# Kernel optimization log

Hardware: AMD Instinct MI355X
Metric: run time of the kernel (lower is better)

The kernel has to match this reference:

```python
import jax, jax.numpy as jnp
import numpy as np

NUM_HEADS = 8
LN_EPS = 1e-5


def setup_inputs() -> dict:
    key = jax.random.key(0)
    ks = jax.random.split(key, 8)
    B, H, W, C = 2, 64, 64, 256
    return {
        "x": jax.random.normal(ks[0], (B, H, W, C), dtype=jnp.float32),
        "cond": jax.random.normal(ks[1], (B, C), dtype=jnp.float32),
        "t": jax.random.randint(ks[2], (B,), 0, 100, dtype=jnp.int64),
        "emb_table": jax.random.normal(ks[3], (100, C), dtype=jnp.float32) * 0.02,
        "ada_w": jax.random.normal(ks[4], (C, 2 * C), dtype=jnp.float32) * 0.02,
        "ada_b": jnp.zeros((2 * C,), dtype=jnp.float32),
        "qkv_w": jax.random.normal(ks[5], (C, 3 * C), dtype=jnp.float32) * 0.02,
        "qkv_b": jnp.zeros((3 * C,), dtype=jnp.float32),
        "proj_w": jax.random.normal(ks[6], (C, C), dtype=jnp.float32) * 0.02,
        "proj_b": jnp.zeros((C,), dtype=jnp.float32),
    }


def reference(x, cond, t, emb_table, ada_w, ada_b, qkv_w, qkv_b, proj_w, proj_b):
    B, H, W, C = x.shape
    N = H * W
    h = NUM_HEADS
    d = C // h
    scale = d ** -0.5

    x = x.reshape(B, N, C)

    # AdaLayerNorm (adalayernorm_abs): timestep embedding -> SiLU -> Linear -> scale/shift
    emb = emb_table[t]                                # [B, C]
    ss = jax.nn.silu(emb) @ ada_w + ada_b             # [B, 2C]
    sc, sh = jnp.split(ss, 2, axis=-1)                # each [B, C]
    mu = jnp.mean(x, axis=-1, keepdims=True)
    var = jnp.var(x, axis=-1, keepdims=True)
    xn = (x - mu) * jax.lax.rsqrt(var + LN_EPS)       # LN without affine
    x = xn * (1.0 + sc[:, None, :]) + sh[:, None, :]

    # QKV projection and head split
    qkv = (x @ qkv_w + qkv_b).reshape(B, N, 3, h, d)
    qkv = jnp.transpose(qkv, (2, 0, 3, 1, 4))          # [3, B, h, N, d]
    q, k, v = qkv[0], qkv[1], qkv[2]

    # Manual attention: full [B, h, N, N] scores (matches original module)
    attn = jnp.einsum('bhnd,bhmd->bhnm', q, k) * scale
    attn = jax.nn.softmax(attn, axis=-1)
    out = jnp.einsum('bhnm,bhmd->bhnd', attn, v)       # [B, h, N, d]
    out = jnp.transpose(out, (0, 2, 1, 3)).reshape(B, N, C)

    out = (out.reshape(B, H, W, C) @ proj_w) + proj_b
    return out
```

## Files before the change

kernel.cpp:

```cpp
#include <hip/hip_runtime.h>
#include <hip/hip_bf16.h>
#include <stdint.h>

typedef __attribute__((ext_vector_type(8))) short bfrag;
typedef __attribute__((ext_vector_type(4))) short bfrag4;
typedef __attribute__((ext_vector_type(4))) float f32x4;
typedef __attribute__((ext_vector_type(2))) float f32x2;
typedef __attribute__((ext_vector_type(2))) unsigned int u32x2;
typedef __attribute__((ext_vector_type(4))) unsigned int u32x4;

__device__ inline short f2bf(float f) {
  union { float f; uint32_t u; } v; v.f = f;
  uint32_t u = v.u;
  uint32_t r = (u + 0x7fffu + ((u >> 16) & 1u)) >> 16;
  return (short)r;
}
__device__ inline float bf2f(short s) {
  return __builtin_bit_cast(float, (uint32_t)((uint32_t)(uint16_t)s << 16));
}

#if __has_builtin(__builtin_amdgcn_cvt_pk_bf16_f32)
typedef __attribute__((ext_vector_type(2))) __bf16 bf16x2_t;
__device__ inline uint32_t pack_bf16(float a, float b) {
  bf16x2_t r = __builtin_amdgcn_cvt_pk_bf16_f32(a, b);
  return __builtin_bit_cast(uint32_t, r);
}
#else
__device__ inline uint32_t pack_bf16(float a, float b) {
  uint32_t ua = __builtin_bit_cast(uint32_t, a) + 0x8000u;
  uint32_t ub = __builtin_bit_cast(uint32_t, b) + 0x8000u;
  return __builtin_amdgcn_perm(ub, ua, 0x07060302);
}
#endif

__device__ inline void lds_barrier() {
  asm volatile("s_waitcnt lgkmcnt(0)" ::: "memory");
  __builtin_amdgcn_s_barrier();
  asm volatile("" ::: "memory");
}

__global__ __launch_bounds__(256) void prep_kernel(
    const float* __restrict__ emb_table, const int* __restrict__ t,
    const float* __restrict__ ada_w, const float* __restrict__ ada_b,
    float* __restrict__ scsh,
    const float* __restrict__ qkv_w, short* __restrict__ qkv_wt,
    const float* __restrict__ proj_w, short* __restrict__ proj_wt) {
  __shared__ float smem[64 * 65];
  const int blk = blockIdx.x;
  const int tid = threadIdx.x;
  if (blk < 16) {
    float* se = smem;
    float* part = smem + 256;
    int b = blk >> 3, ox = blk & 7;
    int tt = t[b];
    float e = emb_table[tt * 256 + tid];
    se[tid] = e / (1.f + __expf(-e));
    __syncthreads();
    int ol = tid & 63, kc = tid >> 6;
    int o = ox * 64 + ol;
    float acc = 0.f;
#pragma unroll 8
    for (int k = kc * 64; k < (kc + 1) * 64; ++k) acc += se[k] * ada_w[k * 512 + o];
    part[tid] = acc;
    __syncthreads();
    if (tid < 64) {
      int oo = ox * 64 + tid;
      scsh[b * 512 + oo] =
          part[tid] + part[64 + tid] + part[128 + tid] + part[192 + tid] + ada_b[oo];
    }
  } else {
    const float* W; short* Wt; int N, lb;
    if (blk < 64) { W = qkv_w; Wt = qkv_wt; N = 768; lb = blk - 16; }
    else          { W = proj_w; Wt = proj_wt; N = 256; lb = blk - 64; }
    float (*tile)[65] = (float(*)[65])smem;
    int k0 = (lb & 3) * 64, n0 = (lb >> 2) * 64;
    int r = tid >> 2, c0 = (tid & 3) * 16;
    const float* src = W + (long)(k0 + r) * N + n0 + c0;
#pragma unroll
    for (int j = 0; j < 16; j += 4) {
      float4 v = *(const float4*)(src + j);
      tile[r][c0 + j] = v.x; tile[r][c0 + j + 1] = v.y;
      tile[r][c0 + j + 2] = v.z; tile[r][c0 + j + 3] = v.w;
    }
    __syncthreads();
    int nl = tid >> 2, kc = (tid & 3) * 16;
    short outv[16];
#pragma unroll
    for (int j = 0; j < 16; ++j) outv[j] = f2bf(tile[kc + j][nl]);
    short* dst = Wt + (long)(n0 + nl) * 256 + k0 + kc;
    *(bfrag*)dst = *(bfrag*)&outv[0];
    *(bfrag*)(dst + 8) = *(bfrag*)&outv[8];
  }
}

__global__ __launch_bounds__(256) void ln_kernel(const float* __restrict__ x,
                                                 const float* __restrict__ scsh,
                                                 short* __restrict__ xb) {
  int row = blockIdx.x * 4 + (threadIdx.x >> 6);
  int b = row >> 12;
  int lane = threadIdx.x & 63;
  float4 v = *(const float4*)(x + (long)row * 256 + lane * 4);
  float s = v.x + v.y + v.z + v.w;
  float sq = v.x * v.x + v.y * v.y + v.z * v.z + v.w * v.w;
#pragma unroll
  for (int off = 32; off > 0; off >>= 1) {
    s += __shfl_xor(s, off);
    sq += __shfl_xor(sq, off);
  }
  float mu = s * (1.f / 256.f);
  float var = sq * (1.f / 256.f) - mu * mu;
  float rstd = rsqrtf(var + 1e-5f);
  const float* scp = scsh + b * 512 + lane * 4;
  float4 sc = *(const float4*)scp;
  float4 sh = *(const float4*)(scp + 256);
  float y0 = (v.x - mu) * rstd * (1.f + sc.x) + sh.x;
  float y1 = (v.y - mu) * rstd * (1.f + sc.y) + sh.y;
  float y2 = (v.z - mu) * rstd * (1.f + sc.z) + sh.z;
  float y3 = (v.w - mu) * rstd * (1.f + sc.w) + sh.w;
  u32x2 o; o.x = pack_bf16(y0, y1); o.y = pack_bf16(y2, y3);
  *(u32x2*)&xb[(long)row * 256 + lane * 4] = o;
}

__global__ __launch_bounds__(256) void gemm_qkv(const short* __restrict__ A,
                                                const short* __restrict__ Bt,
                                                const float* __restrict__ bias,
                                                float qscale,
                                                short* __restrict__ qk,
                                                short* __restrict__ vT) {
  __shared__ short As[128 * 40];
  __shared__ short Bs[64 * 40];
  const int mt = blockIdx.x, nt = blockIdx.y;
  const int tid = threadIdx.x;
  const int w = tid >> 6, lane = tid & 63, l16 = lane & 15, quad = lane >> 4;
  const int ar = tid >> 1, ak = (tid & 1) * 16;
  const int br = tid >> 2, bk = (tid & 3) * 8;
  f32x4 acc[2][4] = {};
  const short* Arow = A + (long)(mt * 128 + ar) * 256 + ak;
  const short* Brow = Bt + (long)(nt * 64 + br) * 256 + bk;
  bfrag a8a = *(const bfrag*)Arow;
  bfrag a8b = *(const bfrag*)(Arow + 8);
  bfrag b8  = *(const bfrag*)Brow;
  for (int kk = 0; kk < 8; ++kk) {
    __syncthreads();
    *(bfrag*)&As[ar * 40 + ak] = a8a;
    *(bfrag*)&As[ar * 40 + ak + 8] = a8b;
    *(bfrag*)&Bs[br * 40 + bk] = b8;
    __syncthreads();
    int kn = (kk < 7) ? (kk + 1) : 7;
    a8a = *(const bfrag*)(Arow + kn * 32);
    a8b = *(const bfrag*)(Arow + kn * 32 + 8);
    b8  = *(const bfrag*)(Brow + kn * 32);
    bfrag a0 = *(const bfrag*)&As[(w * 32 + l16) * 40 + quad * 8];
    bfrag a1 = *(const bfrag*)&As[(w * 32 + 16 + l16) * 40 + quad * 8];
#pragma unroll
    for (int c = 0; c < 4; ++c) {
      bfrag bf = *(const bfrag*)&Bs[(c * 16 + l16) * 40 + quad * 8];
      acc[0][c] = __builtin_amdgcn_mfma_f32_16x16x32_bf16(a0, bf, acc[0][c], 0, 0, 0);
      acc[1][c] = __builtin_amdgcn_mfma_f32_16x16x32_bf16(a1, bf, acc[1][c], 0, 0, 0);
    }
  }
  const int rowb = mt * 128 + w * 32 + quad * 4;
  if (nt < 8) {
#pragma unroll
    for (int rg = 0; rg < 2; ++rg) {
      int row0 = rowb + rg * 16;
#pragma unroll
      for (int c = 0; c < 4; ++c) {
        int col = nt * 64 + c * 16 + l16;
        float bv = bias[col];
        float mult = (col < 256) ? qscale : 1.0f;
#pragma unroll
        for (int r = 0; r < 4; ++r)
          qk[(long)(row0 + r) * 512 + col] = f2bf((acc[rg][c][r] + bv) * mult);
      }
    }
  } else {
    const int bb = mt >> 5;
#pragma unroll
    for (int rg = 0; rg < 2; ++rg) {
      int keyl = (rowb + rg * 16) & 4095;
#pragma unroll
      for (int c = 0; c < 4; ++c) {
        int col = nt * 64 + c * 16 + l16;
        float bv = bias[col];
        int d = col - 512;
        u32x2 dd;
        dd.x = pack_bf16(acc[rg][c][0] + bv, acc[rg][c][1] + bv);
        dd.y = pack_bf16(acc[rg][c][2] + bv, acc[rg][c][3] + bv);
        *(u32x2*)&vT[((long)(bb * 8 + (d >> 5)) * 32 + (d & 31)) * 4096 + keyl] = dd;
      }
    }
  }
}

__global__ __launch_bounds__(256) void attn_kernel(const short* __restrict__ qk,
                                                   const short* __restrict__ vT,
                                                   short* __restrict__ OpB,
                                                   float* __restrict__ lpart) {
  const int bid = blockIdx.x;
  const int c = bid & 7, j = bid >> 3;
  const int bh = c * 2 + (j >> 7);
  const int qt = j & 31;
  const int ks = (j >> 5) & 3;
  const int b = bh >> 3, hh = bh & 7;
  const int tid = threadIdx.x;
  const int w = tid >> 6, lane = tid & 63, l16 = lane & 15, quad = lane >> 4;
  const int sig0 = ((l16 >> 2) * 8) + (l16 & 3);

  __shared__ short Ks[2][128 * 36];
  __shared__ short Vt[2][32 * 132];

  const long rowbase = (long)b * 4096;
  const int qrow0 = qt * 128 + w * 32 + l16;
  bfrag qf[2];
#pragma unroll
  for (int g = 0; g < 2; ++g)
    qf[g] = *(const bfrag*)&qk[(rowbase + qrow0 + g * 16) * 512 + hh * 32 + quad * 8];

  f32x4 olo[2] = {}, ohi[2] = {}, osum[2] = {};
  bfrag vones;
#pragma unroll
  for (int jj = 0; jj < 8; ++jj) vones[jj] = (short)0x3F80;

  const int si = tid >> 2, sk = (tid & 3) * 8;
  const int vrow = tid >> 3, vcol = (tid & 7) * 8;
  const short* ksrc = qk + rowbase * 512 + 256 + hh * 32 + (long)si * 512 + sk;
  const short* vsrc = vT + ((long)bh * 32 + vrow) * 4096 + vcol;

  const int kbase = ks * 1024;
  bfrag k8a = *(const bfrag*)(ksrc + (long)kbase * 512);
  bfrag k8b = *(const bfrag*)(ksrc + (long)(kbase + 64) * 512);
  bfrag v8a = *(const bfrag*)(vsrc + kbase);
  bfrag v8b = *(const bfrag*)(vsrc + kbase + 64);

  int buf = 0;
  for (int i = 0; i < 8; ++i) {
    *(bfrag*)&Ks[buf][si * 36 + sk] = k8a;
    *(bfrag*)&Ks[buf][(si + 64) * 36 + sk] = k8b;
    *(bfrag*)&Vt[buf][vrow * 132 + vcol] = v8a;
    *(bfrag*)&Vt[buf][vrow * 132 + 64 + vcol] = v8b;
    lds_barrier();
    int nn = (i < 7) ? (i + 1) : 7;
    int kb_n = kbase + nn * 128;
    k8a = *(const bfrag*)(ksrc + (long)kb_n * 512);
    k8b = *(const bfrag*)(ksrc + (long)(kb_n + 64) * 512);
    v8a = *(const bfrag*)(vsrc + kb_n);
    v8b = *(const bfrag*)(vsrc + kb_n + 64);

#pragma unroll
    for (int h = 0; h < 2; ++h) {
      const int kb0 = h * 64, kb1 = h * 64 + 32;
      bfrag kA0 = *(const bfrag*)&Ks[buf][(kb0 + sig0) * 36 + quad * 8];
      bfrag kA1 = *(const bfrag*)&Ks[buf][(kb0 + sig0 + 4) * 36 + quad * 8];
      bfrag kB0 = *(const bfrag*)&Ks[buf][(kb1 + sig0) * 36 + quad * 8];
      bfrag kB1 = *(const bfrag*)&Ks[buf][(kb1 + sig0 + 4) * 36 + quad * 8];
      bfrag vAlo = *(const bfrag*)&Vt[buf][l16 * 132 + kb0 + quad * 8];
      bfrag vAhi = *(const bfrag*)&Vt[buf][(16 + l16) * 132 + kb0 + quad * 8];
      bfrag vBlo = *(const bfrag*)&Vt[buf][l16 * 132 + kb1 + quad * 8];
      bfrag vBhi = *(const bfrag*)&Vt[buf][(16 + l16) * 132 + kb1 + quad * 8];
      f32x4 z = {0, 0, 0, 0};
      f32x4 sA0[2], sA1[2], sB0[2], sB1[2];
      __builtin_amdgcn_s_setprio(1);
#pragma unroll
      for (int g = 0; g < 2; ++g) {
        sA0[g] = __builtin_amdgcn_mfma_f32_16x16x32_bf16(kA0, qf[g], z, 0, 0, 0);
        sA1[g] = __builtin_amdgcn_mfma_f32_16x16x32_bf16(kA1, qf[g], z, 0, 0, 0);
        sB0[g] = __builtin_amdgcn_mfma_f32_16x16x32_bf16(kB0, qf[g], z, 0, 0, 0);
        sB1[g] = __builtin_amdgcn_mfma_f32_16x16x32_bf16(kB1, qf[g], z, 0, 0, 0);
      }
      __builtin_amdgcn_s_setprio(0);
      bfrag pbA[2], pbB[2];
#pragma unroll
      for (int g = 0; g < 2; ++g) {
        float a0 = __builtin_amdgcn_exp2f(sA0[g][0]);
        float a1 = __builtin_amdgcn_exp2f(sA0[g][1]);
        float a2 = __builtin_amdgcn_exp2f(sA0[g][2]);
        float a3 = __builtin_amdgcn_exp2f(sA0[g][3]);
        float a4 = __builtin_amdgcn_exp2f(sA1[g][0]);
        float a5 = __builtin_amdgcn_exp2f(sA1[g][1]);
        float a6 = __builtin_amdgcn_exp2f(sA1[g][2]);
        float a7 = __builtin_amdgcn_exp2f(sA1[g][3]);
        float b0 = __builtin_amdgcn_exp2f(sB0[g][0]);
        float b1 = __builtin_amdgcn_exp2f(sB0[g][1]);
        float b2 = __builtin_amdgcn_exp2f(sB0[g][2]);
        float b3 = __builtin_amdgcn_exp2f(sB0[g][3]);
        float b4 = __builtin_amdgcn_exp2f(sB1[g][0]);
        float b5 = __builtin_amdgcn_exp2f(sB1[g][1]);
        float b6 = __builtin_amdgcn_exp2f(sB1[g][2]);
        float b7 = __builtin_amdgcn_exp2f(sB1[g][3]);
        u32x4 pka, pkb;
        pka.x = pack_bf16(a0, a1); pka.y = pack_bf16(a2, a3);
        pka.z = pack_bf16(a4, a5); pka.w = pack_bf16(a6, a7);
        pkb.x = pack_bf16(b0, b1); pkb.y = pack_bf16(b2, b3);
        pkb.z = pack_bf16(b4, b5); pkb.w = pack_bf16(b6, b7);
        pbA[g] = __builtin_bit_cast(bfrag, pka);
        pbB[g] = __builtin_bit_cast(bfrag, pkb);
      }
      __builtin_amdgcn_s_setprio(1);
#pragma unroll
      for (int g = 0; g < 2; ++g) {
        olo[g]  = __builtin_amdgcn_mfma_f32_16x16x32_bf16(pbA[g], vAlo, olo[g], 0, 0, 0);
        ohi[g]  = __builtin_amdgcn_mfma_f32_16x16x32_bf16(pbA[g], vAhi, ohi[g], 0, 0, 0);
        osum[g] = __builtin_amdgcn_mfma_f32_16x16x32_bf16(pbA[g], vones, osum[g], 0, 0, 0);
        olo[g]  = __builtin_amdgcn_mfma_f32_16x16x32_bf16(pbB[g], vBlo, olo[g], 0, 0, 0);
        ohi[g]  = __builtin_amdgcn_mfma_f32_16x16x32_bf16(pbB[g], vBhi, ohi[g], 0, 0, 0);
        osum[g] = __builtin_amdgcn_mfma_f32_16x16x32_bf16(pbB[g], vones, osum[g], 0, 0, 0);
      }
      __builtin_amdgcn_s_setprio(0);
    }
    buf ^= 1;
  }
  uint16_t* Ob = (uint16_t*)OpB;
  const long obase = ((long)ks * 16 + bh) * 4096;
  const int qgb = qt * 128 + w * 32;
#pragma unroll
  for (int g = 0; g < 2; ++g) {
    if (l16 == 0)
      *(f32x4*)&lpart[obase + qgb + g * 16 + quad * 4] = osum[g];
#pragma unroll
    for (int r = 0; r < 4; ++r) {
      int q = qgb + g * 16 + quad * 4 + r;
      uint32_t pk = pack_bf16(olo[g][r], ohi[g][r]);
      Ob[(obase + q) * 32 + l16] = (uint16_t)pk;
      Ob[(obase + q) * 32 + l16 + 16] = (uint16_t)(pk >> 16);
    }
  }
}

__global__ __launch_bounds__(256) void proj_kernel(const short* __restrict__ OpB,
                                                   const float* __restrict__ lpart,
                                                   const short* __restrict__ Bt,
                                                   const float* __restrict__ bias,
                                                   float* __restrict__ out) {
  __shared__ short As[128 * 40];
  __shared__ short Bs[64 * 40];
  const int mt = blockIdx.x, nt = blockIdx.y;
  const int tid = threadIdx.x;
  const int w = tid >> 6, lane = tid & 63, l16 = lane & 15, quad = lane >> 4;
  const int ar = tid >> 1, ak = (tid & 1) * 16;
  const int br = tid >> 2, bk = (tid & 3) * 8;
  f32x4 acc[2][4] = {};

  const int row = mt * 128 + ar;
  const int q = row & 4095, bq = row >> 12;
  const short* Brow = Bt + (long)(nt * 64 + br) * 256 + bk;

  long lb0 = (long)(bq * 8) * 4096 + q;
  bfrag pa[4][2];
  f32x4 pl;
#pragma unroll
  for (int ks = 0; ks < 4; ++ks) {
    long base = (lb0 + (long)ks * 16 * 4096) * 32 + ak;
    pa[ks][0] = *(const bfrag*)&OpB[base];
    pa[ks][1] = *(const bfrag*)&OpB[base + 8];
    pl[ks] = lpart[lb0 + (long)ks * 16 * 4096];
  }
  bfrag b8 = *(const bfrag*)Brow;

  for (int kk = 0; kk < 8; ++kk) {
    float linv = 1.f / (pl[0] + pl[1] + pl[2] + pl[3]);
    short av[16];
#pragma unroll
    for (int h = 0; h < 2; ++h) {
#pragma unroll
      for (int j = 0; j < 8; j += 2) {
        float v0 = (bf2f(pa[0][h][j]) + bf2f(pa[1][h][j]) +
                    bf2f(pa[2][h][j]) + bf2f(pa[3][h][j])) * linv;
        float v1 = (bf2f(pa[0][h][j+1]) + bf2f(pa[1][h][j+1]) +
                    bf2f(pa[2][h][j+1]) + bf2f(pa[3][h][j+1])) * linv;
        *(uint32_t*)&av[h * 8 + j] = pack_bf16(v0, v1);
      }
    }
    __syncthreads();
    *(bfrag*)&As[ar * 40 + ak] = *(bfrag*)&av[0];
    *(bfrag*)&As[ar * 40 + ak + 8] = *(bfrag*)&av[8];
    *(bfrag*)&Bs[br * 40 + bk] = b8;
    __syncthreads();
    int kn = (kk < 7) ? (kk + 1) : 7;
    long lbn = (long)(bq * 8 + kn) * 4096 + q;
#pragma unroll
    for (int ks = 0; ks < 4; ++ks) {
      long base = (lbn + (long)ks * 16 * 4096) * 32 + ak;
      pa[ks][0] = *(const bfrag*)&OpB[base];
      pa[ks][1] = *(const bfrag*)&OpB[base + 8];
      pl[ks] = lpart[lbn + (long)ks * 16 * 4096];
    }
    b8 = *(const bfrag*)(Brow + kn * 32);

    bfrag a0 = *(const bfrag*)&As[(w * 32 + l16) * 40 + quad * 8];
    bfrag a1 = *(const bfrag*)&As[(w * 32 + 16 + l16) * 40 + quad * 8];
#pragma unroll
    for (int c = 0; c < 4; ++c) {
      bfrag bf = *(const bfrag*)&Bs[(c * 16 + l16) * 40 + quad * 8];
      acc[0][c] = __builtin_amdgcn_mfma_f32_16x16x32_bf16(a0, bf, acc[0][c], 0, 0, 0);
      acc[1][c] = __builtin_amdgcn_mfma_f32_16x16x32_bf16(a1, bf, acc[1][c], 0, 0, 0);
    }
  }
  const int rowb = mt * 128 + w * 32 + quad * 4;
#pragma unroll
  for (int rg = 0; rg < 2; ++rg) {
    int row0 = rowb + rg * 16;
#pragma unroll
    for (int c = 0; c < 4; ++c) {
      int col = nt * 64 + c * 16 + l16;
      float bv = bias[col];
#pragma unroll
      for (int r = 0; r < 4; ++r)
        out[(long)(row0 + r) * 256 + col] = acc[rg][c][r] + bv;
    }
  }
}

extern "C" void kernel_launch(void* const* d_in, const int* in_sizes, int n_in,
                              void* d_out, int out_size, void* d_ws, size_t ws_size,
                              hipStream_t stream) {
  const float* x      = (const float*)d_in[0];
  const int*   t      = (const int*)d_in[2];
  const float* emb    = (const float*)d_in[3];
  const float* ada_w  = (const float*)d_in[4];
  const float* ada_b  = (const float*)d_in[5];
  const float* qkv_w  = (const float*)d_in[6];
  const float* qkv_b  = (const float*)d_in[7];
  const float* proj_w = (const float*)d_in[8];
  const float* proj_b = (const float*)d_in[9];

  char* ws = (char*)d_ws;
  float* scsh     = (float*)(ws);
  short* qkv_wt   = (short*)(ws + 4096);
  short* proj_wt  = (short*)(ws + 397312);
  short* xb       = (short*)(ws + 528384);
  short* qk_out   = (short*)(ws + 4722688);
  short* vT       = (short*)(ws + 13111296);
  short* OpB      = (short*)(ws + 21499904);
  float* lpart    = (float*)(ws + 38277120);

  const float QS = 0.17677669529663687f * 1.4426950408889634f;

  prep_kernel<<<80, 256, 0, stream>>>(emb, t, ada_w, ada_b, scsh,
                                      qkv_w, qkv_wt, proj_w, proj_wt);
  ln_kernel<<<2048, 256, 0, stream>>>(x, scsh, xb);
  gemm_qkv<<<dim3(64, 12), 256, 0, stream>>>(xb, qkv_wt, qkv_b, QS, qk_out, vT);
  attn_kernel<<<2048, 256, 0, stream>>>(qk_out, vT, OpB, lpart);
  proj_kernel<<<dim3(64, 4), 256, 0, stream>>>(OpB, lpart, proj_wt, proj_b,
                                               (float*)d_out);
}
```

Measured before the change: 163.2 us.

## Restructure attention K/V double-buffering to one barrier per tile with prefetch-two-ahead

Reworks the attention main loop so the next tile's K/V is written into the alternate LDS buffer in the middle of the current tile's compute, and global loads are issued two tiles ahead. Each iteration now has a single barrier placed at its end rather than a store-then-barrier at its start. The aim is to hide LDS stores and global-load latency behind MFMA and exp work. The cost is more registers held live across the compute and a more intricate buffer-hazard ordering.

```diff
diff --git a/kernel.cpp b/kernel.cpp
--- a/kernel.cpp
+++ b/kernel.cpp
@@ -228,88 +228,102 @@
   const short* vsrc = vT + ((long)bh * 32 + vrow) * 4096 + vcol;
 
   const int kbase = ks * 1024;
-  bfrag k8a = *(const bfrag*)(ksrc + (long)kbase * 512);
-  bfrag k8b = *(const bfrag*)(ksrc + (long)(kbase + 64) * 512);
-  bfrag v8a = *(const bfrag*)(vsrc + kbase);
-  bfrag v8b = *(const bfrag*)(vsrc + kbase + 64);
-
-  int buf = 0;
+  bfrag k8a, k8b, v8a, v8b;
+
+  auto half = [&](const short* KsB, const short* VtB, int h) {
+    const int kb0 = h * 64, kb1 = h * 64 + 32;
+    bfrag kA0 = *(const bfrag*)&KsB[(kb0 + sig0) * 36 + quad * 8];
+    bfrag kA1 = *(const bfrag*)&KsB[(kb0 + sig0 + 4) * 36 + quad * 8];
+    bfrag kB0 = *(const bfrag*)&KsB[(kb1 + sig0) * 36 + quad * 8];
+    bfrag kB1 = *(const bfrag*)&KsB[(kb1 + sig0 + 4) * 36 + quad * 8];
+    bfrag vAlo = *(const bfrag*)&VtB[l16 * 132 + kb0 + quad * 8];
+    bfrag vAhi = *(const bfrag*)&VtB[(16 + l16) * 132 + kb0 + quad * 8];
+    bfrag vBlo = *(const bfrag*)&VtB[l16 * 132 + kb1 + quad * 8];
+    bfrag vBhi = *(const bfrag*)&VtB[(16 + l16) * 132 + kb1 + quad * 8];
+    f32x4 z = {0, 0, 0, 0};
+    f32x4 sA0[2], sA1[2], sB0[2], sB1[2];
+    __builtin_amdgcn_s_setprio(1);
+#pragma unroll
+    for (int g = 0; g < 2; ++g) {
+      sA0[g] = __builtin_amdgcn_mfma_f32_16x16x32_bf16(kA0, qf[g], z, 0, 0, 0);
+      sA1[g] = __builtin_amdgcn_mfma_f32_16x16x32_bf16(kA1, qf[g], z, 0, 0, 0);
+      sB0[g] = __builtin_amdgcn_mfma_f32_16x16x32_bf16(kB0, qf[g], z, 0, 0, 0);
+      sB1[g] = __builtin_amdgcn_mfma_f32_16x16x32_bf16(kB1, qf[g], z, 0, 0, 0);
+    }
+    __builtin_amdgcn_s_setprio(0);
+    bfrag pbA[2], pbB[2];
+#pragma unroll
+    for (int g = 0; g < 2; ++g) {
+      float a0 = __builtin_amdgcn_exp2f(sA0[g][0]);
+      float a1 = __builtin_amdgcn_exp2f(sA0[g][1]);
+      float a2 = __builtin_amdgcn_exp2f(sA0[g][2]);
+      float a3 = __builtin_amdgcn_exp2f(sA0[g][3]);
+      float a4 = __builtin_amdgcn_exp2f(sA1[g][0]);
+      float a5 = __builtin_amdgcn_exp2f(sA1[g][1]);
+      float a6 = __builtin_amdgcn_exp2f(sA1[g][2]);
+      float a7 = __builtin_amdgcn_exp2f(sA1[g][3]);
+      float b0 = __builtin_amdgcn_exp2f(sB0[g][0]);
+      float b1 = __builtin_amdgcn_exp2f(sB0[g][1]);
+      float b2 = __builtin_amdgcn_exp2f(sB0[g][2]);
+      float b3 = __builtin_amdgcn_exp2f(sB0[g][3]);
+      float b4 = __builtin_amdgcn_exp2f(sB1[g][0]);
+      float b5 = __builtin_amdgcn_exp2f(sB1[g][1]);
+      float b6 = __builtin_amdgcn_exp2f(sB1[g][2]);
+      float b7 = __builtin_amdgcn_exp2f(sB1[g][3]);
+      u32x4 pka, pkb;
+      pka.x = pack_bf16(a0, a1); pka.y = pack_bf16(a2, a3);
+      pka.z = pack_bf16(a4, a5); pka.w = pack_bf16(a6, a7);
+      pkb.x = pack_bf16(b0, b1); pkb.y = pack_bf16(b2, b3);
+      pkb.z = pack_bf16(b4, b5); pkb.w = pack_bf16(b6, b7);
+      pbA[g] = __builtin_bit_cast(bfrag, pka);
+      pbB[g] = __builtin_bit_cast(bfrag, pkb);
+    }
+    __builtin_amdgcn_s_setprio(1);
+#pragma unroll
+    for (int g = 0; g < 2; ++g) {
+      olo[g]  = __builtin_amdgcn_mfma_f32_16x16x32_bf16(pbA[g], vAlo, olo[g], 0, 0, 0);
+      ohi[g]  = __builtin_amdgcn_mfma_f32_16x16x32_bf16(pbA[g], vAhi, ohi[g], 0, 0, 0);
+      osum[g] = __builtin_amdgcn_mfma_f32_16x16x32_bf16(pbA[g], vones, osum[g], 0, 0, 0);
+      olo[g]  = __builtin_amdgcn_mfma_f32_16x16x32_bf16(pbB[g], vBlo, olo[g], 0, 0, 0);
+      ohi[g]  = __builtin_amdgcn_mfma_f32_16x16x32_bf16(pbB[g], vBhi, ohi[g], 0, 0, 0);
+      osum[g] = __builtin_amdgcn_mfma_f32_16x16x32_bf16(pbB[g], vones, osum[g], 0, 0, 0);
+    }
+    __builtin_amdgcn_s_setprio(0);
+  };
+
+  k8a = *(const bfrag*)(ksrc + (long)kbase * 512);
+  k8b = *(const bfrag*)(ksrc + (long)(kbase + 64) * 512);
+  v8a = *(const bfrag*)(vsrc + kbase);
+  v8b = *(const bfrag*)(vsrc + kbase + 64);
+  *(bfrag*)&Ks[0][si * 36 + sk] = k8a;
+  *(bfrag*)&Ks[0][(si + 64) * 36 + sk] = k8b;
+  *(bfrag*)&Vt[0][vrow * 132 + vcol] = v8a;
+  *(bfrag*)&Vt[0][vrow * 132 + 64 + vcol] = v8b;
+  lds_barrier();
+  k8a = *(const bfrag*)(ksrc + (long)(kbase + 128) * 512);
+  k8b = *(const bfrag*)(ksrc + (long)(kbase + 192) * 512);
+  v8a = *(const bfrag*)(vsrc + kbase + 128);
+  v8b = *(const bfrag*)(vsrc + kbase + 192);
+
   for (int i = 0; i < 8; ++i) {
-    *(bfrag*)&Ks[buf][si * 36 + sk] = k8a;
-    *(bfrag*)&Ks[buf][(si + 64) * 36 + sk] = k8b;
-    *(bfrag*)&Vt[buf][vrow * 132 + vcol] = v8a;
-    *(bfrag*)&Vt[buf][vrow * 132 + 64 + vcol] = v8b;
+    const int buf = i & 1, nbuf = buf ^ 1;
+    half(Ks[buf], Vt[buf], 0);
+    *(bfrag*)&Ks[nbuf][si * 36 + sk] = k8a;
+    *(bfrag*)&Ks[nbuf][(si + 64) * 36 + sk] = k8b;
+    *(bfrag*)&Vt[nbuf][vrow * 132 + vcol] = v8a;
+    *(bfrag*)&Vt[nbuf][vrow * 132 + 64 + vcol] = v8b;
+    {
+      int nn = (i < 6) ? (i + 2) : 7;
+      int kb_n = kbase + nn * 128;
+      k8a = *(const bfrag*)(ksrc + (long)kb_n * 512);
+      k8b = *(const bfrag*)(ksrc + (long)(kb_n + 64) * 512);
+      v8a = *(const bfrag*)(vsrc + kb_n);
+      v8b = *(const bfrag*)(vsrc + kb_n + 64);
+    }
+    half(Ks[buf], Vt[buf], 1);
     lds_barrier();
-    int nn = (i < 7) ? (i + 1) : 7;
-    int kb_n = kbase + nn * 128;
-    k8a = *(const bfrag*)(ksrc + (long)kb_n * 512);
-    k8b = *(const bfrag*)(ksrc + (long)(kb_n + 64) * 512);
-    v8a = *(const bfrag*)(vsrc + kb_n);
-    v8b = *(const bfrag*)(vsrc + kb_n + 64);
-
-#pragma unroll
-    for (int h = 0; h < 2; ++h) {
-      const int kb0 = h * 64, kb1 = h * 64 + 32;
-      bfrag kA0 = *(const bfrag*)&Ks[buf][(kb0 + sig0) * 36 + quad * 8];
-      bfrag kA1 = *(const bfrag*)&Ks[buf][(kb0 + sig0 + 4) * 36 + quad * 8];
-      bfrag kB0 = *(const bfrag*)&Ks[buf][(kb1 + sig0) * 36 + quad * 8];
-      bfrag kB1 = *(const bfrag*)&Ks[buf][(kb1 + sig0 + 4) * 36 + quad * 8];
-      bfrag vAlo = *(const bfrag*)&Vt[buf][l16 * 132 + kb0 + quad * 8];
-      bfrag vAhi = *(const bfrag*)&Vt[buf][(16 + l16) * 132 + kb0 + quad * 8];
-      bfrag vBlo = *(const bfrag*)&Vt[buf][l16 * 132 + kb1 + quad * 8];
-      bfrag vBhi = *(const bfrag*)&Vt[buf][(16 + l16) * 132 + kb1 + quad * 8];
-      f32x4 z = {0, 0, 0, 0};
-      f32x4 sA0[2], sA1[2], sB0[2], sB1[2];
-      __builtin_amdgcn_s_setprio(1);
-#pragma unroll
-      for (int g = 0; g < 2; ++g) {
-        sA0[g] = __builtin_amdgcn_mfma_f32_16x16x32_bf16(kA0, qf[g], z, 0, 0, 0);
-        sA1[g] = __builtin_amdgcn_mfma_f32_16x16x32_bf16(kA1, qf[g], z, 0, 0, 0);
-        sB0[g] = __builtin_amdgcn_mfma_f32_16x16x32_bf16(kB0, qf[g], z, 0, 0, 0);
-        sB1[g] = __builtin_amdgcn_mfma_f32_16x16x32_bf16(kB1, qf[g], z, 0, 0, 0);
-      }
-      __builtin_amdgcn_s_setprio(0);
-      bfrag pbA[2], pbB[2];
-#pragma unroll
-      for (int g = 0; g < 2; ++g) {
-        float a0 = __builtin_amdgcn_exp2f(sA0[g][0]);
-        float a1 = __builtin_amdgcn_exp2f(sA0[g][1]);
-        float a2 = __builtin_amdgcn_exp2f(sA0[g][2]);
-        float a3 = __builtin_amdgcn_exp2f(sA0[g][3]);
-        float a4 = __builtin_amdgcn_exp2f(sA1[g][0]);
-        float a5 = __builtin_amdgcn_exp2f(sA1[g][1]);
-        float a6 = __builtin_amdgcn_exp2f(sA1[g][2]);
-        float a7 = __builtin_amdgcn_exp2f(sA1[g][3]);
-        float b0 = __builtin_amdgcn_exp2f(sB0[g][0]);
-        float b1 = __builtin_amdgcn_exp2f(sB0[g][1]);
-        float b2 = __builtin_amdgcn_exp2f(sB0[g][2]);
-        float b3 = __builtin_amdgcn_exp2f(sB0[g][3]);
-        float b4 = __builtin_amdgcn_exp2f(sB1[g][0]);
-        float b5 = __builtin_amdgcn_exp2f(sB1[g][1]);
-        float b6 = __builtin_amdgcn_exp2f(sB1[g][2]);
-        float b7 = __builtin_amdgcn_exp2f(sB1[g][3]);
-        u32x4 pka, pkb;
-        pka.x = pack_bf16(a0, a1); pka.y = pack_bf16(a2, a3);
-        pka.z = pack_bf16(a4, a5); pka.w = pack_bf16(a6, a7);
-        pkb.x = pack_bf16(b0, b1); pkb.y = pack_bf16(b2, b3);
-        pkb.z = pack_bf16(b4, b5); pkb.w = pack_bf16(b6, b7);
-        pbA[g] = __builtin_bit_cast(bfrag, pka);
-        pbB[g] = __builtin_bit_cast(bfrag, pkb);
-      }
-      __builtin_amdgcn_s_setprio(1);
-#pragma unroll
-      for (int g = 0; g < 2; ++g) {
-        olo[g]  = __builtin_amdgcn_mfma_f32_16x16x32_bf16(pbA[g], vAlo, olo[g], 0, 0, 0);
-        ohi[g]  = __builtin_amdgcn_mfma_f32_16x16x32_bf16(pbA[g], vAhi, ohi[g], 0, 0, 0);
-        osum[g] = __builtin_amdgcn_mfma_f32_16x16x32_bf16(pbA[g], vones, osum[g], 0, 0, 0);
-        olo[g]  = __builtin_amdgcn_mfma_f32_16x16x32_bf16(pbB[g], vBlo, olo[g], 0, 0, 0);
-        ohi[g]  = __builtin_amdgcn_mfma_f32_16x16x32_bf16(pbB[g], vBhi, ohi[g], 0, 0, 0);
-        osum[g] = __builtin_amdgcn_mfma_f32_16x16x32_bf16(pbB[g], vones, osum[g], 0, 0, 0);
-      }
-      __builtin_amdgcn_s_setprio(0);
-    }
-    buf ^= 1;
-  }
+  }
+
   uint16_t* Ob = (uint16_t*)OpB;
   const long obase = ((long)ks * 16 + bh) * 4096;
   const int qgb = qt * 128 + w * 32;
```

Result: slower. 231.7 us (+41.9%).
